# Kernel tuning notes

Measured on AMD Instinct MI355X. Metric: run time of the kernel, lower is better.

Reference implementation:

```python
import jax, jax.numpy as jnp
import numpy as np

N_NODES = 100000
N_EDGES = 1000000
N_LABEL = 200000
D_IN = 128
D_HID = 128


def setup_inputs() -> dict:
    key = jax.random.key(0)
    k1, k2, k3, k4, k5 = jax.random.split(key, 5)
    node_feature = jax.random.normal(k1, (N_NODES, D_IN), dtype=jnp.float32)
    edge_index = jax.random.randint(k2, (2, N_EDGES), 0, N_NODES, dtype=jnp.int64)
    edge_label_index = jax.random.randint(k3, (2, N_LABEL), 0, N_NODES, dtype=jnp.int64)
    W1 = jax.random.normal(k4, (D_IN, D_HID), dtype=jnp.float32) * (1.0 / np.sqrt(D_IN))
    b1 = jnp.zeros((D_HID,), dtype=jnp.float32)
    W2 = jax.random.normal(k5, (D_HID, D_HID), dtype=jnp.float32) * (1.0 / np.sqrt(D_HID))
    b2 = jnp.zeros((D_HID,), dtype=jnp.float32)
    return {"node_feature": node_feature, "edge_index": edge_index,
            "edge_label_index": edge_label_index,
            "W1": W1, "b1": b1, "W2": W2, "b2": b2}


def reference(node_feature, edge_index, edge_label_index, W1, b1, W2, b2):
    N = node_feature.shape[0]
    # GCN normalization with added self-loops (PyG GCNConv default)
    loop = jnp.arange(N, dtype=edge_index.dtype)
    src = jnp.concatenate([edge_index[0], loop])  # [E+N]
    dst = jnp.concatenate([edge_index[1], loop])  # [E+N]
    deg = jax.ops.segment_sum(jnp.ones_like(dst, dtype=node_feature.dtype), dst, N)
    dinv = jnp.where(deg > 0, jax.lax.rsqrt(deg), 0.0)
    norm = dinv[src] * dinv[dst]  # [E+N]

    def gcn_conv(x, W, b):
        h = x @ W                              # [N, d] transform first (d small)
        msg = h[src] * norm[:, None]           # gather + scale over edges
        return jax.ops.segment_sum(msg, dst, N) + b  # scatter-add to targets

    # eval mode: dropout(p=0.2) is identity
    x = jax.nn.relu(gcn_conv(node_feature, W1, b1))
    x = gcn_conv(x, W2, b2)

    # edge scoring: gather both endpoints, elementwise mul, sum over features
    nodes_first = x[edge_label_index[0]]
    nodes_second = x[edge_label_index[1]]
    pred = jnp.sum(nodes_first * nodes_second, axis=-1)  # [N_LABEL]
    return pred
```

## Files before the change

kernel.cpp:

```cpp
#include <hip/hip_runtime.h>
#include <hip/hip_bf16.h>


#define N_NODES 100000
#define N_EDGES 1000000
#define N_LABEL 200000
#define D_FEAT 128
#define BM 128

#define NB 782
#define BCAP 2048
#define P1_EPT 16
#define P1_BLOCKS 245
#define G_GEMM 782
#define G_CONV 128

typedef short bf16x8 __attribute__((ext_vector_type(8)));
typedef float f32x4 __attribute__((ext_vector_type(4)));

__device__ inline unsigned int f2bf(float x) {
    unsigned int u = __float_as_uint(x);
    return (u + 0x7FFFu + ((u >> 16) & 1u)) >> 16;
}
__device__ inline unsigned int bf16pack(float a, float b) {
    return f2bf(a) | (f2bf(b) << 16);
}
__device__ inline float bflo(unsigned int u) { return __uint_as_float(u << 16); }
__device__ inline float bfhi(unsigned int u) { return __uint_as_float(u & 0xFFFF0000u); }

__global__ __launch_bounds__(256) void w2bf_zero(
    const float* __restrict__ W1, const float* __restrict__ W2,
    unsigned short* __restrict__ Wt1, unsigned short* __restrict__ Wt2,
    int* __restrict__ gcur) {
    int b = blockIdx.x, t = threadIdx.x;
    if (b == G_CONV) {
        ((int4*)gcur)[t] = make_int4(0, 0, 0, 0);
        return;
    }
    int i = b * 256 + t;
    const float* W = (i < 16384) ? W1 : W2;
    unsigned short* Wt = (i < 16384) ? Wt1 : Wt2;
    int j = i & 16383;
    int n = j >> 7, k = j & 127;
    Wt[j] = (unsigned short)f2bf(W[(size_t)k * 128 + n]);
}

template <bool BF16_IN>
__device__ __forceinline__ void gemm_body(const void* __restrict__ Xv,
                                          const unsigned short* __restrict__ Wt,
                                          unsigned int* __restrict__ Y,
                                          int nrows, int bid, short* Ws) {
    int t = threadIdx.x;
#pragma unroll
    for (int i = 0; i < 8; ++i) {
        int c = i * 256 + t;
        int n = c >> 4, q = c & 15;
        uint4 v = *(const uint4*)&Wt[(size_t)n * 128 + q * 8];
        *(uint4*)&Ws[n * 128 + ((q ^ (n & 15)) << 3)] = v;
    }
    __syncthreads();

    int wv = t >> 6;
    int lane = t & 63, l16 = lane & 15, quad = lane >> 4;
    int rbase = bid * BM + wv * 32;

    f32x4 acc[2][8];
#pragma unroll
    for (int rt = 0; rt < 2; ++rt)
#pragma unroll
        for (int nt = 0; nt < 8; ++nt) acc[rt][nt] = (f32x4){0.f, 0.f, 0.f, 0.f};

#pragma unroll
    for (int kb = 0; kb < 4; ++kb) {
        bf16x8 af[2];
#pragma unroll
        for (int rt = 0; rt < 2; ++rt) {
            int row = rbase + rt * 16 + l16;
            if (row > nrows - 1) row = nrows - 1;
            if constexpr (BF16_IN) {
                const unsigned int* Xb = (const unsigned int*)Xv;
                af[rt] = *(const bf16x8*)&Xb[(size_t)row * 64 + kb * 16 + quad * 4];
            } else {
                const float* X = (const float*)Xv;
                float4 fa = ((const float4*)X)[(size_t)row * 32 + kb * 8 + quad * 2];
                float4 fb = ((const float4*)X)[(size_t)row * 32 + kb * 8 + quad * 2 + 1];
                union { uint4 u; bf16x8 v; } cv;
                cv.u.x = bf16pack(fa.x, fa.y);
                cv.u.y = bf16pack(fa.z, fa.w);
                cv.u.z = bf16pack(fb.x, fb.y);
                cv.u.w = bf16pack(fb.z, fb.w);
                af[rt] = cv.v;
            }
        }
        bf16x8 bfr[8];
#pragma unroll
        for (int nt = 0; nt < 8; ++nt) {
            int n = nt * 16 + l16;
            bfr[nt] = *(const bf16x8*)&Ws[n * 128 + (((kb * 4 + quad) ^ l16) << 3)];
        }
#pragma unroll
        for (int rt = 0; rt < 2; ++rt)
#pragma unroll
            for (int nt = 0; nt < 8; ++nt)
                acc[rt][nt] = __builtin_amdgcn_mfma_f32_16x16x32_bf16(
                    af[rt], bfr[nt], acc[rt][nt], 0, 0, 0);
    }

    short* Ys = (short*)Y;
#pragma unroll
    for (int rt = 0; rt < 2; ++rt)
#pragma unroll
        for (int reg = 0; reg < 4; ++reg) {
            int row = rbase + rt * 16 + quad * 4 + reg;
            if (row < nrows) {
#pragma unroll
                for (int nt = 0; nt < 8; ++nt)
                    Ys[(size_t)row * 128 + nt * 16 + l16] = (short)f2bf(acc[rt][nt][reg]);
            }
        }
}

__global__ __launch_bounds__(256) void gemm128_mfma_bf16(const unsigned int* __restrict__ Xb,
                                                         const unsigned short* __restrict__ Wt,
                                                         unsigned int* __restrict__ Y,
                                                         int nrows) {
    __shared__ __align__(16) short Ws[128 * 128];
    gemm_body<true>(Xb, Wt, Y, nrows, blockIdx.x, Ws);
}

__global__ __launch_bounds__(256) void fused_gemm1_pass1(
    const float* __restrict__ feat, const unsigned short* __restrict__ wt1,
    unsigned int* __restrict__ Hb,
    const int* __restrict__ src, const int* __restrict__ dst,
    int* __restrict__ gcur, unsigned int* __restrict__ temp) {
    __shared__ __align__(16) short Ws[128 * 128];
    int b = blockIdx.x, t = threadIdx.x;
    if (b < G_GEMM) {
        gemm_body<false>(feat, wt1, Hb, N_NODES, b, Ws);
        return;
    }
    b -= G_GEMM;
    int* hist = (int*)Ws;
    int* base = hist + NB;
    for (int i = t; i < NB; i += 256) hist[i] = 0;
    __syncthreads();

    int se[P1_EPT], de[P1_EPT], rk[P1_EPT];
    int e0 = b * (P1_EPT * 256) + t;
#pragma unroll
    for (int j = 0; j < P1_EPT; ++j) {
        int e = e0 + j * 256;
        if (e < N_EDGES) {
            se[j] = src[e];
            de[j] = dst[e];
            rk[j] = atomicAdd(&hist[de[j] >> 7], 1);
        }
    }
    __syncthreads();
    for (int i = t; i < NB; i += 256) {
        int h = hist[i];
        base[i] = h ? atomicAdd(&gcur[i], h) : 0;
    }
    __syncthreads();
#pragma unroll
    for (int j = 0; j < P1_EPT; ++j) {
        int e = e0 + j * 256;
        if (e < N_EDGES) {
            int k = de[j] >> 7;
            int pos = base[k] + rk[j];
            if (pos < BCAP)
                temp[(size_t)k * BCAP + pos] =
                    (unsigned int)(((de[j] & 127) << 17) | se[j]);
        }
    }
}

__global__ __launch_bounds__(256) void pass2_sort(
    const int* __restrict__ gcur, const unsigned int* __restrict__ temp,
    int* __restrict__ row_ptr, float* __restrict__ dinv,
    int* __restrict__ packed) {
    int k = blockIdx.x, t = threadIdx.x;
    __shared__ unsigned int ed[BCAP];
    __shared__ int hist[128], rp[128], cur[128], sc[128];
    __shared__ int red[256];

    int part = 0;
    for (int j = t; j < NB; j += 256)
        if (j < k) part += gcur[j];
    red[t] = part;
    __syncthreads();
    for (int off = 128; off > 0; off >>= 1) {
        if (t < off) red[t] += red[t + off];
        __syncthreads();
    }
    int gbase = red[0];
    int nk = gcur[k];
    if (nk > BCAP) nk = BCAP;

    if (t < 128) { hist[t] = 0; cur[t] = 0; }
    __syncthreads();
    for (int i = t; i < nk; i += 256) {
        unsigned int v = temp[(size_t)k * BCAP + i];
        ed[i] = v;
        atomicAdd(&hist[v >> 17], 1);
    }
    __syncthreads();

    if (t < 128) sc[t] = hist[t];
    __syncthreads();
    for (int off = 1; off < 128; off <<= 1) {
        int a = (t < 128 && t >= off) ? sc[t - off] : 0;
        __syncthreads();
        if (t < 128) sc[t] += a;
        __syncthreads();
    }
    if (t < 128) {
        rp[t] = sc[t] - hist[t];
        int n = k * 128 + t;
        if (n < N_NODES) {
            row_ptr[n] = gbase + rp[t];
            dinv[n] = rsqrtf((float)(hist[t] + 1));
        }
    }
    if (k == NB - 1 && t == 0) row_ptr[N_NODES] = N_EDGES;
    __syncthreads();

    for (int i = t; i < nk; i += 256) {
        unsigned int v = ed[i];
        int dl = v >> 17;
        int r = atomicAdd(&cur[dl], 1);
        packed[gbase + rp[dl] + r] = (int)(v & 0x1FFFF);
    }
}

template <bool RELU>
__global__ __launch_bounds__(256) void aggregate(const unsigned int* __restrict__ Hb,
                                                 const int* __restrict__ packed,
                                                 const int* __restrict__ row_ptr,
                                                 const float* __restrict__ dinv,
                                                 const float* __restrict__ bias,
                                                 unsigned int* __restrict__ Xb) {
    int v0 = blockIdx.x * 8 + (threadIdx.x >> 6) * 2;
    int v1 = v0 + 1;
    int lane = threadIdx.x & 63;
    if (v0 >= N_NODES) return;
    bool h1 = (v1 < N_NODES);

    int st0 = row_ptr[v0], en0 = row_ptr[v0 + 1];
    int st1 = h1 ? row_ptr[v1] : 0, en1 = h1 ? row_ptr[v1 + 1] : 0;
    float dv0 = dinv[v0];
    float dv1 = h1 ? dinv[v1] : 0.f;

    unsigned int su0 = Hb[(size_t)v0 * 64 + lane];
    float a0 = dv0 * bflo(su0), a1 = dv0 * bfhi(su0);
    unsigned int su1 = h1 ? Hb[(size_t)v1 * 64 + lane] : 0u;
    float b0 = dv1 * bflo(su1), b1 = dv1 * bfhi(su1);

    int p = 0;
    if (lane < 32) {
        if (st0 + lane < en0) p = packed[st0 + lane];
    } else {
        if (st1 + lane - 32 < en1) p = packed[st1 + lane - 32];
    }

    for (int c0 = st0, c1 = st1; c0 < en0 || c1 < en1; c0 += 32, c1 += 32) {
        int n0 = en0 - c0; n0 = n0 < 0 ? 0 : (n0 > 32 ? 32 : n0);
        int n1 = en1 - c1; n1 = n1 < 0 ? 0 : (n1 > 32 ? 32 : n1);
        bool act = (lane < 32) ? (lane < n0) : (lane - 32 < n1);
        float dld = dinv[p];
        float d = act ? dld : 0.f;

        int nmax = n0 > n1 ? n0 : n1;
        int pn = 0;
        bool pref = false;
        for (int j = 0; j < nmax; j += 8) {
            int sA[8], sB[8];
#pragma unroll
            for (int q = 0; q < 8; ++q) {
                sA[q] = __shfl(p, j + q);
                sB[q] = __shfl(p, 32 + j + q);
            }
            unsigned int uA[8], uB[8];
#pragma unroll
            for (int q = 0; q < 8; ++q) {
                uA[q] = Hb[(size_t)sA[q] * 64 + lane];
                uB[q] = Hb[(size_t)sB[q] * 64 + lane];
            }
            if (!pref) {
                pref = true;
                if (lane < 32) {
                    if (c0 + 32 + lane < en0) pn = packed[c0 + 32 + lane];
                } else {
                    if (c1 + lane < en1) pn = packed[c1 + lane];
                }
            }
            float dA[8], dB[8];
#pragma unroll
            for (int q = 0; q < 8; ++q) {
                dA[q] = __shfl(d, j + q);
                dB[q] = __shfl(d, 32 + j + q);
            }
#pragma unroll
            for (int q = 0; q < 8; ++q) {
                a0 = fmaf(dA[q], bflo(uA[q]), a0);
                a1 = fmaf(dA[q], bfhi(uA[q]), a1);
                b0 = fmaf(dB[q], bflo(uB[q]), b0);
                b1 = fmaf(dB[q], bfhi(uB[q]), b1);
            }
        }
        p = pn;
    }

    float2 bb = ((const float2*)bias)[lane];
    a0 = fmaf(a0, dv0, bb.x);
    a1 = fmaf(a1, dv0, bb.y);
    b0 = fmaf(b0, dv1, bb.x);
    b1 = fmaf(b1, dv1, bb.y);
    if (RELU) {
        a0 = fmaxf(a0, 0.f);
        a1 = fmaxf(a1, 0.f);
        b0 = fmaxf(b0, 0.f);
        b1 = fmaxf(b1, 0.f);
    }
    Xb[(size_t)v0 * 64 + lane] = bf16pack(a0, a1);
    if (h1) Xb[(size_t)v1 * 64 + lane] = bf16pack(b0, b1);
}

__global__ __launch_bounds__(256) void score_kernel(const int* __restrict__ ea,
                                                    const int* __restrict__ eb,
                                                    const unsigned int* __restrict__ Xb,
                                                    float* __restrict__ out) {
    int wbase = (blockIdx.x * 4 + (threadIdx.x >> 6)) * 4;
    int lane = threadIdx.x & 63;
    if (wbase >= N_LABEL) return;
    int ne = N_LABEL - wbase;
    if (ne > 4) ne = 4;

    unsigned int ua[4], ub[4];
#pragma unroll
    for (int e = 0; e < 4; ++e)
        if (e < ne) {
            int ia = ea[wbase + e], ib = eb[wbase + e];
            ua[e] = Xb[(size_t)ia * 64 + lane];
            ub[e] = Xb[(size_t)ib * 64 + lane];
        }
#pragma unroll
    for (int e = 0; e < 4; ++e)
        if (e < ne) {
            float p = bflo(ua[e]) * bflo(ub[e]) + bfhi(ua[e]) * bfhi(ub[e]);
#pragma unroll
            for (int off = 32; off > 0; off >>= 1) p += __shfl_down(p, off);
            if (lane == 0) out[wbase + e] = p;
        }
}

extern "C" void kernel_launch(void* const* d_in, const int* in_sizes, int n_in,
                              void* d_out, int out_size, void* d_ws, size_t ws_size,
                              hipStream_t stream) {
    const float* feat = (const float*)d_in[0];
    const int* ei = (const int*)d_in[1];
    const int* eli = (const int*)d_in[2];
    const float* W1 = (const float*)d_in[3];
    const float* b1 = (const float*)d_in[4];
    const float* W2 = (const float*)d_in[5];
    const float* b2 = (const float*)d_in[6];
    float* out = (float*)d_out;

    const int* src = ei;
    const int* dst = ei + N_EDGES;
    const int* la = eli;
    const int* lb = eli + N_LABEL;

    int* gcur = (int*)d_ws;
    int* row_ptr = gcur + 1024;
    float* dinv = (float*)(row_ptr + N_NODES + 4);
    unsigned short* wt1 = (unsigned short*)(dinv + N_NODES);
    unsigned short* wt2 = wt1 + 16384;
    int* packed = (int*)(wt2 + 16384);
    unsigned int* Hb = (unsigned int*)(packed + N_EDGES);
    unsigned int* Xb = Hb + (size_t)N_NODES * 64;
    unsigned int* temp = Xb;

    const int TB = 256;
    int gGemm = (N_NODES + BM - 1) / BM;
    int gAgg = (N_NODES + 7) / 8;
    int gScore = (N_LABEL + 15) / 16;

    w2bf_zero<<<G_CONV + 1, TB, 0, stream>>>(W1, W2, wt1, wt2, gcur);

    fused_gemm1_pass1<<<G_GEMM + P1_BLOCKS, TB, 0, stream>>>(
        feat, wt1, Hb, src, dst, gcur, temp);

    pass2_sort<<<NB, TB, 0, stream>>>(gcur, temp, row_ptr, dinv, packed);

    aggregate<true><<<gAgg, TB, 0, stream>>>(Hb, packed, row_ptr, dinv, b1, Xb);

    gemm128_mfma_bf16<<<gGemm, TB, 0, stream>>>(Xb, wt2, Hb, N_NODES);
    aggregate<false><<<gAgg, TB, 0, stream>>>(Hb, packed, row_ptr, dinv, b2, Xb);

    score_kernel<<<gScore, TB, 0, stream>>>(la, lb, Xb, out);
}
```

Baseline: 279.4 us.

## Replace global-atomic bucketing with per-block local sort and offset table

Pass1 blocks now sort their 4096 edges locally by destination bucket in shared memory and write them out contiguously, along with a per-block bucket offset table, instead of claiming slots in global buckets through atomics on a shared counter array. Pass2 reads each block's segment for its bucket through the offset table and a prefix scan. This removes the global atomics and the gcur zeroing, and the write to temp becomes coalesced. In exchange, pass2 does a strided per-thread serial copy that reads scattered short segments from 245 sources, which may be uncoalesced and load-imbalanced.

Result: no change. 278.4 us (-0.3%).

```diff
diff --git a/kernel.cpp b/kernel.cpp
--- a/kernel.cpp
+++ b/kernel.cpp
@@ -28,16 +28,10 @@
 __device__ inline float bflo(unsigned int u) { return __uint_as_float(u << 16); }
 __device__ inline float bfhi(unsigned int u) { return __uint_as_float(u & 0xFFFF0000u); }
 
-__global__ __launch_bounds__(256) void w2bf_zero(
+__global__ __launch_bounds__(256) void w2bf(
     const float* __restrict__ W1, const float* __restrict__ W2,
-    unsigned short* __restrict__ Wt1, unsigned short* __restrict__ Wt2,
-    int* __restrict__ gcur) {
-    int b = blockIdx.x, t = threadIdx.x;
-    if (b == G_CONV) {
-        ((int4*)gcur)[t] = make_int4(0, 0, 0, 0);
-        return;
-    }
-    int i = b * 256 + t;
+    unsigned short* __restrict__ Wt1, unsigned short* __restrict__ Wt2) {
+    int i = blockIdx.x * 256 + threadIdx.x;
     const float* W = (i < 16384) ? W1 : W2;
     unsigned short* Wt = (i < 16384) ? Wt1 : Wt2;
     int j = i & 16383;
@@ -132,7 +126,7 @@
     const float* __restrict__ feat, const unsigned short* __restrict__ wt1,
     unsigned int* __restrict__ Hb,
     const int* __restrict__ src, const int* __restrict__ dst,
-    int* __restrict__ gcur, unsigned int* __restrict__ temp) {
+    unsigned int* __restrict__ temp, int* __restrict__ bofs) {
     __shared__ __align__(16) short Ws[128 * 128];
     int b = blockIdx.x, t = threadIdx.x;
     if (b < G_GEMM) {
@@ -140,13 +134,15 @@
         return;
     }
     b -= G_GEMM;
-    int* hist = (int*)Ws;
-    int* base = hist + NB;
-    for (int i = t; i < NB; i += 256) hist[i] = 0;
+    unsigned int* ed16 = (unsigned int*)Ws;
+    int* hist = (int*)(ed16 + 4096);
+    int* red = hist + 1024;
+
+    for (int i = t; i < 1024; i += 256) hist[i] = 0;
     __syncthreads();
 
     int se[P1_EPT], de[P1_EPT], rk[P1_EPT];
-    int e0 = b * (P1_EPT * 256) + t;
+    int e0 = b * 4096 + t;
 #pragma unroll
     for (int j = 0; j < P1_EPT; ++j) {
         int e = e0 + j * 256;
@@ -157,65 +153,99 @@
         }
     }
     __syncthreads();
-    for (int i = t; i < NB; i += 256) {
-        int h = hist[i];
-        base[i] = h ? atomicAdd(&gcur[i], h) : 0;
-    }
-    __syncthreads();
+
+    int c0 = hist[4 * t], c1 = hist[4 * t + 1], c2 = hist[4 * t + 2], c3 = hist[4 * t + 3];
+    int s = c0 + c1 + c2 + c3;
+    red[t] = s;
+    __syncthreads();
+    for (int off = 1; off < 256; off <<= 1) {
+        int a = (t >= off) ? red[t - off] : 0;
+        __syncthreads();
+        red[t] += a;
+        __syncthreads();
+    }
+    int excl = red[t] - s;
+    hist[4 * t] = excl;
+    hist[4 * t + 1] = excl + c0;
+    hist[4 * t + 2] = excl + c0 + c1;
+    hist[4 * t + 3] = excl + c0 + c1 + c2;
+    __syncthreads();
+
 #pragma unroll
     for (int j = 0; j < P1_EPT; ++j) {
         int e = e0 + j * 256;
         if (e < N_EDGES) {
-            int k = de[j] >> 7;
-            int pos = base[k] + rk[j];
-            if (pos < BCAP)
-                temp[(size_t)k * BCAP + pos] =
-                    (unsigned int)(((de[j] & 127) << 17) | se[j]);
-        }
+            int pos = hist[de[j] >> 7] + rk[j];
+            ed16[pos] = (unsigned int)(((de[j] & 127) << 17) | se[j]);
+        }
+    }
+    __syncthreads();
+
+#pragma unroll
+    for (int i = 0; i < 4; ++i)
+        ((uint4*)temp)[(size_t)b * 1024 + i * 256 + t] = ((uint4*)ed16)[i * 256 + t];
+    for (int j = t; j < NB; j += 256) bofs[b * (NB + 1) + j] = hist[j];
+    if (t == 0) {
+        int cnt = N_EDGES - b * 4096;
+        if (cnt > 4096) cnt = 4096;
+        bofs[b * (NB + 1) + NB] = cnt;
     }
 }
 
 __global__ __launch_bounds__(256) void pass2_sort(
-    const int* __restrict__ gcur, const unsigned int* __restrict__ temp,
+    const unsigned int* __restrict__ temp, const int* __restrict__ bofs,
     int* __restrict__ row_ptr, float* __restrict__ dinv,
     int* __restrict__ packed) {
     int k = blockIdx.x, t = threadIdx.x;
     __shared__ unsigned int ed[BCAP];
-    __shared__ int hist[128], rp[128], cur[128], sc[128];
-    __shared__ int red[256];
-
-    int part = 0;
-    for (int j = t; j < NB; j += 256)
-        if (j < k) part += gcur[j];
-    red[t] = part;
+    __shared__ int hist[128], rp[128], cur[128], sc2[128];
+    __shared__ int red[256], sc[256];
+
+    int s_t = 0, len = 0;
+    if (t < P1_BLOCKS) {
+        s_t = bofs[t * (NB + 1) + k];
+        len = bofs[t * (NB + 1) + k + 1] - s_t;
+    }
+    red[t] = s_t;
     __syncthreads();
     for (int off = 128; off > 0; off >>= 1) {
         if (t < off) red[t] += red[t + off];
         __syncthreads();
     }
     int gbase = red[0];
-    int nk = gcur[k];
+    __syncthreads();
+    sc[t] = len;
+    __syncthreads();
+    for (int off = 1; off < 256; off <<= 1) {
+        int a = (t >= off) ? sc[t - off] : 0;
+        __syncthreads();
+        sc[t] += a;
+        __syncthreads();
+    }
+    int dloc = sc[t] - len;
+    int nk = sc[255];
     if (nk > BCAP) nk = BCAP;
 
     if (t < 128) { hist[t] = 0; cur[t] = 0; }
     __syncthreads();
-    for (int i = t; i < nk; i += 256) {
-        unsigned int v = temp[(size_t)k * BCAP + i];
-        ed[i] = v;
-        atomicAdd(&hist[v >> 17], 1);
-    }
-    __syncthreads();
-
-    if (t < 128) sc[t] = hist[t];
+    for (int i = 0; i < len; ++i) {
+        int d = dloc + i;
+        if (d < BCAP) ed[d] = temp[(size_t)t * 4096 + s_t + i];
+    }
+    __syncthreads();
+    for (int i = t; i < nk; i += 256) atomicAdd(&hist[ed[i] >> 17], 1);
+    __syncthreads();
+
+    if (t < 128) sc2[t] = hist[t];
     __syncthreads();
     for (int off = 1; off < 128; off <<= 1) {
-        int a = (t < 128 && t >= off) ? sc[t - off] : 0;
-        __syncthreads();
-        if (t < 128) sc[t] += a;
+        int a = (t < 128 && t >= off) ? sc2[t - off] : 0;
+        __syncthreads();
+        if (t < 128) sc2[t] += a;
         __syncthreads();
     }
     if (t < 128) {
-        rp[t] = sc[t] - hist[t];
+        rp[t] = sc2[t] - hist[t];
         int n = k * 128 + t;
         if (n < N_NODES) {
             row_ptr[n] = gbase + rp[t];
@@ -371,8 +401,7 @@
     const int* la = eli;
     const int* lb = eli + N_LABEL;
 
-    int* gcur = (int*)d_ws;
-    int* row_ptr = gcur + 1024;
+    int* row_ptr = (int*)d_ws;
     float* dinv = (float*)(row_ptr + N_NODES + 4);
     unsigned short* wt1 = (unsigned short*)(dinv + N_NODES);
     unsigned short* wt2 = wt1 + 16384;
@@ -380,18 +409,19 @@
     unsigned int* Hb = (unsigned int*)(packed + N_EDGES);
     unsigned int* Xb = Hb + (size_t)N_NODES * 64;
     unsigned int* temp = Xb;
+    int* bofs = (int*)(temp + (size_t)P1_BLOCKS * 4096);
 
     const int TB = 256;
     int gGemm = (N_NODES + BM - 1) / BM;
     int gAgg = (N_NODES + 7) / 8;
     int gScore = (N_LABEL + 15) / 16;
 
-    w2bf_zero<<<G_CONV + 1, TB, 0, stream>>>(W1, W2, wt1, wt2, gcur);
+    w2bf<<<G_CONV, TB, 0, stream>>>(W1, W2, wt1, wt2);
 
     fused_gemm1_pass1<<<G_GEMM + P1_BLOCKS, TB, 0, stream>>>(
-        feat, wt1, Hb, src, dst, gcur, temp);
-
-    pass2_sort<<<NB, TB, 0, stream>>>(gcur, temp, row_ptr, dinv, packed);
+        feat, wt1, Hb, src, dst, temp, bofs);
+
+    pass2_sort<<<NB, TB, 0, stream>>>(temp, bofs, row_ptr, dinv, packed);
 
     aggregate<true><<<gAgg, TB, 0, stream>>>(Hb, packed, row_ptr, dinv, b1, Xb);
 
```
